# Kernel tuning notes

Hardware: AMD Instinct MI355X
Metric: run time of the kernel (lower is better)

## Reference

```python
import jax, jax.numpy as jnp
import numpy as np

B, Q, K = 16, 64, 1024
QS = KS = VS = 256
H = 128
NEG = -1e6


def setup_inputs() -> dict:
    key = jax.random.key(0)
    ks = jax.random.split(key, 7)
    queries = jax.random.normal(ks[0], (B, Q, QS), dtype=jnp.float32)
    keys = jax.random.normal(ks[1], (B, K, KS), dtype=jnp.float32)
    values = jax.random.normal(ks[2], (B, K, VS), dtype=jnp.float32)
    valid_len = jax.random.randint(ks[3], (B,), 0, 512, dtype=jnp.int64)
    # Linear weights (PyTorch Linear stores (out, in); we store (in, out) for x @ W)
    Wq = jax.random.normal(ks[4], (QS, H), dtype=jnp.float32) / np.sqrt(QS)
    Wk = jax.random.normal(ks[5], (KS, H), dtype=jnp.float32) / np.sqrt(KS)
    Ws = jax.random.normal(ks[6], (H,), dtype=jnp.float32) / np.sqrt(H)
    return {"queries": queries, "keys": keys, "values": values,
            "valid_len": valid_len, "Wq": Wq, "Wk": Wk, "Ws": Ws}


def reference(queries, keys, values, valid_len, Wq, Wk, Ws):
    q = jnp.einsum('bqe,eh->bqh', queries, Wq)          # (B,Q,H)
    k = jnp.einsum('bke,eh->bkh', keys, Wk)             # (B,K,H)
    features = jnp.tanh(q[:, :, None, :] + k[:, None, :, :])  # (B,Q,K,H)
    scores = jnp.einsum('bqkh,h->bqk', features, Ws)    # (B,Q,K)
    # front_mask=True: mask the FIRST valid_len[b] key positions
    pos = jnp.arange(K)
    valid = pos[None, None, :] >= valid_len[:, None, None]  # (B,1,K)
    scores = jnp.where(valid, scores, NEG)
    attn = jax.nn.softmax(scores, axis=-1)              # (B,Q,K)
    return jnp.einsum('bqk,bkv->bqv', attn, values)     # (B,Q,VS)
```

## Files before the change

kernel.cpp:

```cpp
#include <hip/hip_runtime.h>

#define NB 16
#define NQ 64
#define NK 1024
#define ES 256
#define NH 128
#define VS 256
#define SCALE2 2.885390081777927f
#define L2E    1.4426950408889634f

__device__ __forceinline__ float exp2_fast(float x) {
    float r; asm("v_exp_f32 %0, %1" : "=v"(r) : "v"(x)); return r;
}
__device__ __forceinline__ float rcp_fast(float x) {
    float r; asm("v_rcp_f32 %0, %1" : "=v"(r) : "v"(x)); return r;
}
__device__ __forceinline__ void fma4(float4& acc, const float4& wv, float s) {
    acc.x = fmaf(wv.x, s, acc.x);
    acc.y = fmaf(wv.y, s, acc.y);
    acc.z = fmaf(wv.z, s, acc.z);
    acc.w = fmaf(wv.w, s, acc.w);
}

__global__ __launch_bounds__(256) void proj_kernel(
    const float* __restrict__ queries, const float* __restrict__ keys,
    const float* __restrict__ Wq, const float* __restrict__ Wk,
    float* __restrict__ qp, float* __restrict__ kp)
{
    __shared__ __align__(16) float x_lds[32 * 256];
    const int bi  = blockIdx.x;
    const int tid = threadIdx.x;

    const float* src; const float* W; float* dst;
    if (bi < 32) {
        src = queries + (size_t)bi * 32 * ES;
        W   = Wq;
        dst = qp + (size_t)bi * 32 * NH;
    } else {
        const int r0 = (bi - 32) * 32;
        src = keys + (size_t)r0 * ES;
        W   = Wk;
        dst = kp + (size_t)r0 * NH;
    }

    const float4* s4 = (const float4*)src;
    float4* x4 = (float4*)x_lds;
#pragma unroll
    for (int i = 0; i < 8; ++i) x4[tid + i * 256] = s4[tid + i * 256];
    __syncthreads();

    const int h4 = tid & 31;
    const int g  = tid >> 5;
    const float* x0 = x_lds + (g +  0) * 256;
    const float* x1 = x_lds + (g +  8) * 256;
    const float* x2 = x_lds + (g + 16) * 256;
    const float* x3 = x_lds + (g + 24) * 256;

    float4 a0 = {0,0,0,0}, a1 = {0,0,0,0}, a2 = {0,0,0,0}, a3 = {0,0,0,0};
#pragma unroll 4
    for (int e = 0; e < 256; e += 4) {
        const float4 v0 = *(const float4*)(x0 + e);
        const float4 v1 = *(const float4*)(x1 + e);
        const float4 v2 = *(const float4*)(x2 + e);
        const float4 v3 = *(const float4*)(x3 + e);
#pragma unroll
        for (int j = 0; j < 4; ++j) {
            const float4 w4 = *(const float4*)(W + (size_t)(e + j) * NH + h4 * 4);
            const float f0 = (j==0)?v0.x:(j==1)?v0.y:(j==2)?v0.z:v0.w;
            const float f1 = (j==0)?v1.x:(j==1)?v1.y:(j==2)?v1.z:v1.w;
            const float f2 = (j==0)?v2.x:(j==1)?v2.y:(j==2)?v2.z:v2.w;
            const float f3 = (j==0)?v3.x:(j==1)?v3.y:(j==2)?v3.z:v3.w;
            fma4(a0, w4, f0); fma4(a1, w4, f1);
            fma4(a2, w4, f2); fma4(a3, w4, f3);
        }
    }
    const float c = SCALE2;
    float4 o;
    o.x=a0.x*c; o.y=a0.y*c; o.z=a0.z*c; o.w=a0.w*c;
    *(float4*)(dst + (size_t)(g +  0) * NH + h4 * 4) = o;
    o.x=a1.x*c; o.y=a1.y*c; o.z=a1.z*c; o.w=a1.w*c;
    *(float4*)(dst + (size_t)(g +  8) * NH + h4 * 4) = o;
    o.x=a2.x*c; o.y=a2.y*c; o.z=a2.z*c; o.w=a2.w*c;
    *(float4*)(dst + (size_t)(g + 16) * NH + h4 * 4) = o;
    o.x=a3.x*c; o.y=a3.y*c; o.z=a3.z*c; o.w=a3.w*c;
    *(float4*)(dst + (size_t)(g + 24) * NH + h4 * 4) = o;
}

__global__ __launch_bounds__(256, 4) void scores_kernel(
    const float* __restrict__ qp, const float* __restrict__ kp,
    const float* __restrict__ Ws, const int* __restrict__ valid_len,
    float* __restrict__ pT)
{
    __shared__ __align__(16) float kp_s[64 * 128];
    __shared__ __align__(16) float qp_s[8 * 128];
    __shared__ __align__(16) float ws_s[128];

    const int kt  = blockIdx.x;
    const int qt  = blockIdx.y;
    const int b   = blockIdx.z;
    const int tid = threadIdx.x;
    const int lane = tid & 63;
    const int w    = tid >> 6;
    const int kg   = kt * 64 + lane;
    const int vl   = valid_len[b];

    if (kt * 64 + 63 < vl) {
        pT[((size_t)b * NK + kg) * NQ + qt * 8 + w]     = 0.0f;
        pT[((size_t)b * NK + kg) * NQ + qt * 8 + w + 4] = 0.0f;
        return;
    }

    const float4* ksrc = (const float4*)(kp + (size_t)(b * NK + kt * 64) * NH);
#pragma unroll
    for (int i = 0; i < 8; ++i) {
        const int idx = tid + i * 256;
        const int row = idx >> 5, c = idx & 31;
        const float4 v = ksrc[idx];
        *(float4*)(kp_s + row * 128 + 4 * (c ^ (row & 7))) = v;
    }
    ((float4*)qp_s)[tid & 255] = ((const float4*)(qp + (size_t)(b * NQ + qt * 8) * NH))[tid & 255];
    if (tid < 32) {
        float4 t = ((const float4*)Ws)[tid];
        t.x *= -2.f; t.y *= -2.f; t.z *= -2.f; t.w *= -2.f;
        ((float4*)ws_s)[tid] = t;
    }
    __syncthreads();

    float sw = ws_s[lane] + ws_s[lane + 64];
#pragma unroll
    for (int off = 32; off; off >>= 1) sw += __shfl_xor(sw, off);
    const float sW = -0.5f * sw;

    const float* qa = qp_s + w * 128;
    const float* qb = qp_s + (w + 4) * 128;
    const float* kr = kp_s + lane * 128;
    const int sw_x = lane & 7;

    float s0 = 0.f, s1 = 0.f;
#pragma unroll 4
    for (int c = 0; c < 32; ++c) {
        const float4 kv = *(const float4*)(kr + 4 * (c ^ sw_x));
        const float4 va = *(const float4*)(qa + 4 * c);
        const float4 vb = *(const float4*)(qb + 4 * c);
        const float4 wv = *(const float4*)(ws_s + 4 * c);
        {
            const float u0 = 1.0f + exp2_fast(va.x + kv.x);
            const float u1 = 1.0f + exp2_fast(va.y + kv.y);
            const float u2 = 1.0f + exp2_fast(va.z + kv.z);
            const float u3 = 1.0f + exp2_fast(va.w + kv.w);
            const float d01 = u0 * u1, d23 = u2 * u3;
            const float n01 = fmaf(wv.y, u0, wv.x * u1);
            const float n23 = fmaf(wv.w, u2, wv.z * u3);
            const float n   = fmaf(n23, d01, n01 * d23);
            s0 = fmaf(n, rcp_fast(d01 * d23), s0);
        }
        {
            const float u0 = 1.0f + exp2_fast(vb.x + kv.x);
            const float u1 = 1.0f + exp2_fast(vb.y + kv.y);
            const float u2 = 1.0f + exp2_fast(vb.z + kv.z);
            const float u3 = 1.0f + exp2_fast(vb.w + kv.w);
            const float d01 = u0 * u1, d23 = u2 * u3;
            const float n01 = fmaf(wv.y, u0, wv.x * u1);
            const float n23 = fmaf(wv.w, u2, wv.z * u3);
            const float n   = fmaf(n23, d01, n01 * d23);
            s1 = fmaf(n, rcp_fast(d01 * d23), s1);
        }
    }

    const float p0 = (kg >= vl) ? exp2_fast((sW + s0) * L2E) : 0.0f;
    const float p1 = (kg >= vl) ? exp2_fast((sW + s1) * L2E) : 0.0f;
    pT[((size_t)b * NK + kg) * NQ + qt * 8 + w]     = p0;
    pT[((size_t)b * NK + kg) * NQ + qt * 8 + w + 4] = p1;
}

__global__ __launch_bounds__(256) void pv_kernel(
    const float* __restrict__ pT, const float* __restrict__ values,
    const int* __restrict__ valid_len,
    float* __restrict__ part, float* __restrict__ zpart)
{
    __shared__ __align__(16) float a_s[128][36];
    __shared__ float zp_s[4][32];
    const int kt  = blockIdx.x;
    const int qh  = blockIdx.y;
    const int b   = blockIdx.z;
    const int tid = threadIdx.x;

    const int vl = valid_len[b];
    if (kt * 128 + 127 < vl) {
        if (tid < 32) zpart[((size_t)kt * NB + b) * NQ + qh * 32 + tid] = 0.f;
#pragma unroll
        for (int q = 0; q < 32; ++q)
            part[(((size_t)kt * NB + b) * NQ + qh * 32 + q) * VS + tid] = 0.f;
        return;
    }

    {
        const int q4 = (tid & 7) * 4;
        const int k0 = tid >> 3;
#pragma unroll
        for (int i = 0; i < 4; ++i) {
            const int k = k0 + 32 * i;
            const float4 v = *(const float4*)(
                pT + ((size_t)b * NK + kt * 128 + k) * NQ + qh * 32 + q4);
            *(float4*)(&a_s[k][q4]) = v;
        }
    }
    __syncthreads();

    {
        const int lane = tid & 63;
        const int w    = tid >> 6;
        const int qq   = lane & 31;
        float z = 0.f;
#pragma unroll
        for (int i = 0; i < 32; ++i) z += a_s[w * 32 + i][qq];
        if (lane < 32) zp_s[w][qq] = z;
    }
    __syncthreads();
    if (tid < 32) {
        const float zf = zp_s[0][tid] + zp_s[1][tid] + zp_s[2][tid] + zp_s[3][tid];
        zpart[((size_t)kt * NB + b) * NQ + qh * 32 + tid] = zf;
    }

    float acc[32];
#pragma unroll
    for (int i = 0; i < 32; ++i) acc[i] = 0.f;

    const float* vb = values + ((size_t)b * NK + kt * 128) * VS + tid;
#pragma unroll 4
    for (int k = 0; k < 128; ++k) {
        const float v = vb[(size_t)k * VS];
#pragma unroll
        for (int j = 0; j < 8; ++j) {
            const float4 a = *(const float4*)(&a_s[k][4 * j]);
            acc[4*j+0] = fmaf(a.x, v, acc[4*j+0]);
            acc[4*j+1] = fmaf(a.y, v, acc[4*j+1]);
            acc[4*j+2] = fmaf(a.z, v, acc[4*j+2]);
            acc[4*j+3] = fmaf(a.w, v, acc[4*j+3]);
        }
    }
#pragma unroll
    for (int q = 0; q < 32; ++q)
        part[(((size_t)kt * NB + b) * NQ + qh * 32 + q) * VS + tid] = acc[q];
}

__global__ __launch_bounds__(256) void finish_kernel(
    const float* __restrict__ part, const float* __restrict__ zpart,
    float* __restrict__ out)
{
    const int r   = blockIdx.x;
    const int tid = threadIdx.x;
    const int b = r >> 6, q = r & 63;
    float z = 0.f, s = 0.f;
#pragma unroll
    for (int kt = 0; kt < 8; ++kt) {
        z += zpart[((size_t)kt * NB + b) * NQ + q];
        s += part[(((size_t)kt * NB + b) * NQ + q) * VS + tid];
    }
    out[(size_t)r * VS + tid] = s / z;
}

extern "C" void kernel_launch(void* const* d_in, const int* in_sizes, int n_in,
                              void* d_out, int out_size, void* d_ws, size_t ws_size,
                              hipStream_t stream)
{
    (void)in_sizes; (void)n_in; (void)out_size; (void)ws_size;
    const float* queries = (const float*)d_in[0];
    const float* keys    = (const float*)d_in[1];
    const float* values  = (const float*)d_in[2];
    const int*   vlen    = (const int*)d_in[3];
    const float* Wq      = (const float*)d_in[4];
    const float* Wk      = (const float*)d_in[5];
    const float* Ws      = (const float*)d_in[6];
    float* out = (float*)d_out;

    float* qp    = (float*)d_ws;
    float* kp    = qp + 131072;
    float* part  = kp;
    float* pT    = kp + 2097152;
    float* zpart = pT + 1048576;

    proj_kernel<<<544, 256, 0, stream>>>(queries, keys, Wq, Wk, qp, kp);
    scores_kernel<<<dim3(16, 8, 16), 256, 0, stream>>>(qp, kp, Ws, vlen, pT);
    pv_kernel<<<dim3(8, 2, 16), 256, 0, stream>>>(pT, values, vlen, part, zpart);
    finish_kernel<<<1024, 256, 0, stream>>>(part, zpart, out);
}
```

Before: 165.4 us.

## Software-pipeline W loads in projection and split PV over finer key tiles

The projection kernel now holds weight rows in registers and prefetches the next eight rows while the current ones feed the FMAs, with occupancy hints added to launch bounds. The PV kernel cuts its key tile from 128 to 64 rows, doubling the grid to 512 blocks for better CU occupancy and finer skipping of masked tiles. The partial-sum buffer moves past zpart to make room for 16 partials. The cost is twice the partial traffic and twice the reduction work in the finish kernel.

```diff
diff --git a/kernel.cpp b/kernel.cpp
--- a/kernel.cpp
+++ b/kernel.cpp
@@ -6,6 +6,7 @@
 #define ES 256
 #define NH 128
 #define VS 256
+#define KT 16
 #define SCALE2 2.885390081777927f
 #define L2E    1.4426950408889634f
 
@@ -22,7 +23,7 @@
     acc.w = fmaf(wv.w, s, acc.w);
 }
 
-__global__ __launch_bounds__(256) void proj_kernel(
+__global__ __launch_bounds__(256, 2) void proj_kernel(
     const float* __restrict__ queries, const float* __restrict__ keys,
     const float* __restrict__ Wq, const float* __restrict__ Wk,
     float* __restrict__ qp, float* __restrict__ kp)
@@ -55,25 +56,67 @@
     const float* x1 = x_lds + (g +  8) * 256;
     const float* x2 = x_lds + (g + 16) * 256;
     const float* x3 = x_lds + (g + 24) * 256;
+    const float* Wc = W + h4 * 4;
 
     float4 a0 = {0,0,0,0}, a1 = {0,0,0,0}, a2 = {0,0,0,0}, a3 = {0,0,0,0};
-#pragma unroll 4
-    for (int e = 0; e < 256; e += 4) {
-        const float4 v0 = *(const float4*)(x0 + e);
-        const float4 v1 = *(const float4*)(x1 + e);
-        const float4 v2 = *(const float4*)(x2 + e);
-        const float4 v3 = *(const float4*)(x3 + e);
-#pragma unroll
-        for (int j = 0; j < 4; ++j) {
-            const float4 w4 = *(const float4*)(W + (size_t)(e + j) * NH + h4 * 4);
-            const float f0 = (j==0)?v0.x:(j==1)?v0.y:(j==2)?v0.z:v0.w;
-            const float f1 = (j==0)?v1.x:(j==1)?v1.y:(j==2)?v1.z:v1.w;
-            const float f2 = (j==0)?v2.x:(j==1)?v2.y:(j==2)?v2.z:v2.w;
-            const float f3 = (j==0)?v3.x:(j==1)?v3.y:(j==2)?v3.z:v3.w;
-            fma4(a0, w4, f0); fma4(a1, w4, f1);
-            fma4(a2, w4, f2); fma4(a3, w4, f3);
-        }
-    }
+
+    float4 wa0, wa1, wa2, wa3, wb0, wb1, wb2, wb3;
+    wa0 = *(const float4*)(Wc + (size_t)0 * NH);
+    wa1 = *(const float4*)(Wc + (size_t)1 * NH);
+    wa2 = *(const float4*)(Wc + (size_t)2 * NH);
+    wa3 = *(const float4*)(Wc + (size_t)3 * NH);
+    wb0 = *(const float4*)(Wc + (size_t)4 * NH);
+    wb1 = *(const float4*)(Wc + (size_t)5 * NH);
+    wb2 = *(const float4*)(Wc + (size_t)6 * NH);
+    wb3 = *(const float4*)(Wc + (size_t)7 * NH);
+
+#define PROJ_PHASE(WREG0, WREG1, WREG2, WREG3, EOFF)                         \
+    {                                                                        \
+        const float4 va = *(const float4*)(x0 + (EOFF));                     \
+        const float4 vb = *(const float4*)(x1 + (EOFF));                     \
+        const float4 vc = *(const float4*)(x2 + (EOFF));                     \
+        const float4 vd = *(const float4*)(x3 + (EOFF));                     \
+        fma4(a0, WREG0, va.x); fma4(a1, WREG0, vb.x);                        \
+        fma4(a2, WREG0, vc.x); fma4(a3, WREG0, vd.x);                        \
+        fma4(a0, WREG1, va.y); fma4(a1, WREG1, vb.y);                        \
+        fma4(a2, WREG1, vc.y); fma4(a3, WREG1, vd.y);                        \
+        fma4(a0, WREG2, va.z); fma4(a1, WREG2, vb.z);                        \
+        fma4(a2, WREG2, vc.z); fma4(a3, WREG2, vd.z);                        \
+        fma4(a0, WREG3, va.w); fma4(a1, WREG3, vb.w);                        \
+        fma4(a2, WREG3, vc.w); fma4(a3, WREG3, vd.w);                        \
+    }
+
+#pragma unroll 1
+    for (int e = 0; e < 240; e += 8) {
+        float4 t0 = *(const float4*)(Wc + (size_t)(e +  8) * NH);
+        float4 t1 = *(const float4*)(Wc + (size_t)(e +  9) * NH);
+        float4 t2 = *(const float4*)(Wc + (size_t)(e + 10) * NH);
+        float4 t3 = *(const float4*)(Wc + (size_t)(e + 11) * NH);
+        PROJ_PHASE(wa0, wa1, wa2, wa3, e);
+        wa0 = t0; wa1 = t1; wa2 = t2; wa3 = t3;
+        t0 = *(const float4*)(Wc + (size_t)(e + 12) * NH);
+        t1 = *(const float4*)(Wc + (size_t)(e + 13) * NH);
+        t2 = *(const float4*)(Wc + (size_t)(e + 14) * NH);
+        t3 = *(const float4*)(Wc + (size_t)(e + 15) * NH);
+        PROJ_PHASE(wb0, wb1, wb2, wb3, e + 4);
+        wb0 = t0; wb1 = t1; wb2 = t2; wb3 = t3;
+    }
+    PROJ_PHASE(wa0, wa1, wa2, wa3, 240);
+    PROJ_PHASE(wb0, wb1, wb2, wb3, 244);
+    {
+        float4 t0 = *(const float4*)(Wc + (size_t)248 * NH);
+        float4 t1 = *(const float4*)(Wc + (size_t)249 * NH);
+        float4 t2 = *(const float4*)(Wc + (size_t)250 * NH);
+        float4 t3 = *(const float4*)(Wc + (size_t)251 * NH);
+        PROJ_PHASE(t0, t1, t2, t3, 248);
+        t0 = *(const float4*)(Wc + (size_t)252 * NH);
+        t1 = *(const float4*)(Wc + (size_t)253 * NH);
+        t2 = *(const float4*)(Wc + (size_t)254 * NH);
+        t3 = *(const float4*)(Wc + (size_t)255 * NH);
+        PROJ_PHASE(t0, t1, t2, t3, 252);
+    }
+#undef PROJ_PHASE
+
     const float c = SCALE2;
     float4 o;
     o.x=a0.x*c; o.y=a0.y*c; o.z=a0.z*c; o.w=a0.w*c;
@@ -178,7 +221,7 @@
     const int* __restrict__ valid_len,
     float* __restrict__ part, float* __restrict__ zpart)
 {
-    __shared__ __align__(16) float a_s[128][36];
+    __shared__ __align__(16) float a_s[64][36];
     __shared__ float zp_s[4][32];
     const int kt  = blockIdx.x;
     const int qh  = blockIdx.y;
@@ -186,7 +229,7 @@
     const int tid = threadIdx.x;
 
     const int vl = valid_len[b];
-    if (kt * 128 + 127 < vl) {
+    if (kt * 64 + 63 < vl) {
         if (tid < 32) zpart[((size_t)kt * NB + b) * NQ + qh * 32 + tid] = 0.f;
 #pragma unroll
         for (int q = 0; q < 32; ++q)
@@ -198,10 +241,10 @@
         const int q4 = (tid & 7) * 4;
         const int k0 = tid >> 3;
 #pragma unroll
-        for (int i = 0; i < 4; ++i) {
+        for (int i = 0; i < 2; ++i) {
             const int k = k0 + 32 * i;
             const float4 v = *(const float4*)(
-                pT + ((size_t)b * NK + kt * 128 + k) * NQ + qh * 32 + q4);
+                pT + ((size_t)b * NK + kt * 64 + k) * NQ + qh * 32 + q4);
             *(float4*)(&a_s[k][q4]) = v;
         }
     }
@@ -213,7 +256,7 @@
         const int qq   = lane & 31;
         float z = 0.f;
 #pragma unroll
-        for (int i = 0; i < 32; ++i) z += a_s[w * 32 + i][qq];
+        for (int i = 0; i < 16; ++i) z += a_s[w * 16 + i][qq];
         if (lane < 32) zp_s[w][qq] = z;
     }
     __syncthreads();
@@ -226,9 +269,9 @@
 #pragma unroll
     for (int i = 0; i < 32; ++i) acc[i] = 0.f;
 
-    const float* vb = values + ((size_t)b * NK + kt * 128) * VS + tid;
+    const float* vb = values + ((size_t)b * NK + kt * 64) * VS + tid;
 #pragma unroll 4
-    for (int k = 0; k < 128; ++k) {
+    for (int k = 0; k < 64; ++k) {
         const float v = vb[(size_t)k * VS];
 #pragma unroll
         for (int j = 0; j < 8; ++j) {
@@ -253,7 +296,7 @@
     const int b = r >> 6, q = r & 63;
     float z = 0.f, s = 0.f;
 #pragma unroll
-    for (int kt = 0; kt < 8; ++kt) {
+    for (int kt = 0; kt < KT; ++kt) {
         z += zpart[((size_t)kt * NB + b) * NQ + q];
         s += part[(((size_t)kt * NB + b) * NQ + q) * VS + tid];
     }
@@ -276,12 +319,12 @@
 
     float* qp    = (float*)d_ws;
     float* kp    = qp + 131072;
-    float* part  = kp;
     float* pT    = kp + 2097152;
     float* zpart = pT + 1048576;
+    float* part  = zpart + 16384;
 
     proj_kernel<<<544, 256, 0, stream>>>(queries, keys, Wq, Wk, qp, kp);
     scores_kernel<<<dim3(16, 8, 16), 256, 0, stream>>>(qp, kp, Ws, vlen, pT);
-    pv_kernel<<<dim3(8, 2, 16), 256, 0, stream>>>(pT, values, vlen, part, zpart);
+    pv_kernel<<<dim3(KT, 2, 16), 256, 0, stream>>>(pT, values, vlen, part, zpart);
     finish_kernel<<<1024, 256, 0, stream>>>(part, zpart, out);
 }
```

Measured after the change: 154.6 us. -6.5%, faster.
